# Kernel optimization log

Hardware: AMD Instinct MI355X
Metric: run time of the kernel (lower is better)

Reference implementation:

```python
import jax, jax.numpy as jnp
import numpy as np

V, E, HD, T, B, S = 32000, 256, 512, 9, 64, 512
H = HD // 2
PAD = 0
NEG = -10000.0


def setup_inputs() -> dict:
    key = jax.random.key(0)
    ks = jax.random.split(key, 12)
    # right-padded variable-length sequences (pack_padded_sequence semantics)
    lengths = jax.random.randint(ks[0], (B,), S // 4, S + 1)
    attention_mask = jnp.arange(S)[None, :] < lengths[:, None]  # [B,S] bool
    input_ids = jax.random.randint(ks[1], (B, S), 1, V)
    input_ids = jnp.where(attention_mask, input_ids, 0)
    sc = 1.0 / np.sqrt(H)
    embed_table = jax.random.normal(ks[2], (V, E), jnp.float32) * 0.02
    embed_table = embed_table.at[PAD].set(0.0)  # padding_idx=0
    u = lambda k, shp: jax.random.uniform(k, shp, jnp.float32, -sc, sc)
    Wih_f, Whh_f, b_f = u(ks[3], (4 * H, E)), u(ks[4], (4 * H, H)), u(ks[5], (4 * H,))
    Wih_r, Whh_r, b_r = u(ks[6], (4 * H, E)), u(ks[7], (4 * H, H)), u(ks[8], (4 * H,))
    W_out, b_out = u(ks[9], (T, HD)), u(ks[10], (T,))
    transitions = jax.random.normal(ks[11], (T, T), jnp.float32)
    transitions = transitions.at[PAD, :].set(NEG).at[:, PAD].set(NEG)
    return dict(input_ids=input_ids, attention_mask=attention_mask,
                embed_table=embed_table, Wih_f=Wih_f, Whh_f=Whh_f, b_f=b_f,
                Wih_r=Wih_r, Whh_r=Whh_r, b_r=b_r, W_out=W_out, b_out=b_out,
                transitions=transitions)


def _lstm_dir(x, m, Wih, Whh, b, reverse):
    """x: [S,B,E] time-major, m: [S,B] bool. Returns h outputs [S,B,H].
    Masked steps freeze (h,c), matching packed-sequence behavior for
    right-padded inputs in both scan directions."""
    Hh = Whh.shape[1]
    def step(carry, inp):
        h, c = carry
        xt, mt = inp
        g = xt @ Wih.T + h @ Whh.T + b                    # [B,4H]
        i, f, gg, o = jnp.split(g, 4, axis=-1)            # torch gate order i,f,g,o
        cn = jax.nn.sigmoid(f) * c + jax.nn.sigmoid(i) * jnp.tanh(gg)
        hn = jax.nn.sigmoid(o) * jnp.tanh(cn)
        mt = mt[:, None]
        return (jnp.where(mt, hn, h), jnp.where(mt, cn, c)), jnp.where(mt, hn, h)
    h0 = jnp.zeros((x.shape[1], Hh), x.dtype)
    _, hs = jax.lax.scan(step, (h0, h0), (x, m), reverse=reverse)
    return hs


def reference(input_ids, attention_mask, embed_table, Wih_f, Whh_f, b_f,
              Wih_r, Whh_r, b_r, W_out, b_out, transitions):
    mask = attention_mask.astype(bool)
    x = embed_table[input_ids].transpose(1, 0, 2)         # [S,B,E] time-major
    m = mask.T                                            # [S,B]
    hf = _lstm_dir(x, m, Wih_f, Whh_f, b_f, reverse=False)
    hr = _lstm_dir(x, m, Wih_r, Whh_r, b_r, reverse=True)
    hs = jnp.concatenate([hf, hr], axis=-1) * m[:, :, None]  # zero pads (pad_packed)
    feats = hs @ W_out.T + b_out                          # [S,B,T]
    # Viterbi forward pass
    v0 = jnp.full((feats.shape[1], T), NEG, feats.dtype).at[:, PAD].set(0.0)
    def vstep(v, inp):
        f_t, m_t = inp
        scores = v[:, :, None] + transitions[None]        # [B, from, to]
        bp = jnp.argmax(scores, axis=1)                   # [B,T]
        best = jnp.take_along_axis(scores, bp[:, None, :], axis=1)[:, 0, :] + f_t
        return jnp.where(m_t[:, None], best, v), bp
    v, bps = jax.lax.scan(vstep, v0, (feats, m))          # bps [S,B,T]
    last = jnp.argmax(v + transitions[PAD], axis=1)       # [B]
    # backtrace: path[i] = where(mask[i+1], bp[i+1][path[i+1]], 0)
    def bstep(tag, inp):
        bp_t, m_t = inp
        prev = jnp.take_along_axis(bp_t, tag[:, None], axis=1)[:, 0]
        prev = jnp.where(m_t, prev, 0)
        return prev, prev
    _, path_rest = jax.lax.scan(bstep, last, (bps[1:], m[1:]), reverse=True)
    return jnp.concatenate([path_rest, last[None]], axis=0).T  # [B,S]
```

## Files before the change

kernel.cpp:

```cpp
#include <hip/hip_runtime.h>


#define SLEN 512
#define NTAG 9
#define NEGV -10000.0f

typedef float f32x2 __attribute__((ext_vector_type(2)));
typedef float f32x4 __attribute__((ext_vector_type(4)));

__device__ __forceinline__ float qsum(float v){
  int t = __builtin_amdgcn_update_dpp(0, __float_as_int(v), 0xB1, 0xF, 0xF, false);
  v += __int_as_float(t);
  t = __builtin_amdgcn_update_dpp(0, __float_as_int(v), 0x4E, 0xF, 0xF, false);
  return v + __int_as_float(t);
}
__device__ __forceinline__ float rsum16(float v){
  v = qsum(v);
  int t = __builtin_amdgcn_update_dpp(0, __float_as_int(v), 0x124, 0xF, 0xF, false);
  v += __int_as_float(t);
  t = __builtin_amdgcn_update_dpp(0, __float_as_int(v), 0x128, 0xF, 0xF, false);
  return v + __int_as_float(t);
}

#define MAC2(S, WP, HV) { \
  f32x2 _h01{(HV).x,(HV).y}, _h23{(HV).z,(HV).w}; \
  asm("v_pk_fma_f32 %0, %1, %2, %0 op_sel:[0,0,0] op_sel_hi:[0,1,1]" : "+v"(S) : "v"(WP), "v"(_h01)); \
  asm("v_pk_fma_f32 %0, %1, %2, %0 op_sel:[1,0,0] op_sel_hi:[1,1,1]" : "+v"(S) : "v"(WP), "v"(_h23)); }

#define LDW(rr,kq,A,B) { f32x4 v = wp[((rr)*4+(kq))*1024 + t]; A = f32x2{v.x,v.y}; B = f32x2{v.z,v.w}; }

#define DECLW \
  f32x2 w00,w01,w02,w03,w04,w05,w06,w07; \
  f32x2 w10,w11,w12,w13,w14,w15,w16,w17; \
  f32x2 w20,w21,w22,w23,w24,w25,w26,w27; \
  f32x2 w30,w31,w32,w33,w34,w35,w36,w37; \
  LDW(0,0,w00,w01) LDW(0,1,w02,w03) LDW(0,2,w04,w05) LDW(0,3,w06,w07) \
  LDW(1,0,w10,w11) LDW(1,1,w12,w13) LDW(1,2,w14,w15) LDW(1,3,w16,w17) \
  LDW(2,0,w20,w21) LDW(2,1,w22,w23) LDW(2,2,w24,w25) LDW(2,3,w26,w27) \
  LDW(3,0,w30,w31) LDW(3,1,w32,w33) LDW(3,2,w34,w35) LDW(3,3,w36,w37)

#define PINW \
  asm volatile("" : "+v"(w00),"+v"(w01),"+v"(w02),"+v"(w03),"+v"(w04),"+v"(w05),"+v"(w06),"+v"(w07)); \
  asm volatile("" : "+v"(w10),"+v"(w11),"+v"(w12),"+v"(w13),"+v"(w14),"+v"(w15),"+v"(w16),"+v"(w17)); \
  asm volatile("" : "+v"(w20),"+v"(w21),"+v"(w22),"+v"(w23),"+v"(w24),"+v"(w25),"+v"(w26),"+v"(w27)); \
  asm volatile("" : "+v"(w30),"+v"(w31),"+v"(w32),"+v"(w33),"+v"(w34),"+v"(w35),"+v"(w36),"+v"(w37));

#define GCHUNK(c, WA0,WA1, WB0,WB1, WC0,WC1, WD0,WD1) { \
  f32x4 hA = *(const f32x4*)(hb + (c)*8); \
  f32x4 hB = *(const f32x4*)(hb + (c)*8 + 4); \
  MAC2(s0,WA0,hA) MAC2(s0,WA1,hB) \
  MAC2(s1,WB0,hA) MAC2(s1,WB1,hB) \
  MAC2(s2,WC0,hA) MAC2(s2,WC1,hB) \
  MAC2(s3,WD0,hA) MAC2(s3,WD1,hB) }

#define GEMV4x16 \
  f32x2 s0{0.f,0.f}, s1{0.f,0.f}, s2{0.f,0.f}, s3{0.f,0.f}; \
  GCHUNK(0, w00,w01, w10,w11, w20,w21, w30,w31) \
  GCHUNK(1, w02,w03, w12,w13, w22,w23, w32,w33) \
  GCHUNK(2, w04,w05, w14,w15, w24,w25, w34,w35) \
  GCHUNK(3, w06,w07, w16,w17, w26,w27, w36,w37)

union PK { struct { float v; int tg; } s; unsigned long long u; };

__global__ void prep_k(const float* __restrict__ wihf, const float* __restrict__ whhf,
                       const float* __restrict__ wihr, const float* __restrict__ whhr,
                       float* __restrict__ wS){
  for (int i = blockIdx.x*blockDim.x + threadIdx.x; i < (1<<20); i += gridDim.x*blockDim.x){
    int e=i&3, t=(i>>2)&1023, inst=(i>>12)&15, g=(i>>16)&3, d=(i>>18)&1, role=(i>>19)&1;
    int rr = inst>>2, kq = inst&3;
    int row = g*256 + (t>>4)*4 + rr;
    int k   = (t&15)*16 + kq*4 + e;
    const float* s = role ? (d? whhr : whhf) : (d? wihr : wihf);
    wS[i] = s[row*256 + k];
  }
}

__global__ __launch_bounds__(1024)
__attribute__((amdgpu_waves_per_eu(4,4)))
void xproj_k(
    int c0, int Sc,
    const int* __restrict__ ids, const float* __restrict__ embed,
    const float* __restrict__ wS,
    const float* __restrict__ bias_f, const float* __restrict__ bias_r,
    float* __restrict__ xg, long xg_par_str)
{
  __shared__ __align__(16) float xbig[64][576];
  __shared__ int ids_l[1024];
  const int t = threadIdx.x;
  const int bid = blockIdx.x;
  const int bp = bid & 31, g = (bid>>5)&3, d = bid>>7;
  const int rg = t>>4, ks = t&15;
  const int e = ks&3, bu = (ks>>2)&1;

  const f32x4* wp = (const f32x4*)(wS + (long)((d*4+g)*16)*4096);
  DECLW
  PINW
  const float bbr = (d ? bias_r : bias_f)[g*256 + rg*4 + e];

  for (int i=t; i<2*Sc; i+=1024){
    int b = (i>=Sc) ? 1 : 0, sp = i - b*Sc;
    int sg = d ? (SLEN-1-(c0*Sc+sp)) : (c0*Sc+sp);
    ids_l[i] = ids[(bp*2+b)*SLEN + sg];
  }
  const int SH = (Sc < 64) ? Sc : 64;
  float* xgb = xg + (long)(c0&1)*xg_par_str;

  for (int sp0=0; sp0<Sc; sp0+=SH){
    __syncthreads();
    for (int c = t; c < SH*128; c += 1024){
      int ss = c>>7, b = (c>>6)&1, kk = c&63;
      int sp = sp0 + ss;
      f32x4 v = ((const f32x4*)embed)[(long)ids_l[b*Sc+sp]*64 + kk];
      float* xb = &xbig[ss][(kk>>2)*36 + (kk&3)*8 + b];
      xb[0] = v.x; xb[2] = v.y; xb[4] = v.z; xb[6] = v.w;
    }
    __syncthreads();
    for (int sp=sp0; sp<sp0+SH; sp++){
      const float* hb = &xbig[sp-sp0][ks*36];
      GEMV4x16
      float r0a = rsum16(s0.x), r0b = rsum16(s0.y);
      float r1a = rsum16(s1.x), r1b = rsum16(s1.y);
      float r2a = rsum16(s2.x), r2b = rsum16(s2.y);
      float r3a = rsum16(s3.x), r3b = rsum16(s3.y);
      if (ks < 8){
        float va = (e==0)?r0a:(e==1)?r1a:(e==2)?r2a:r3a;
        float vb = (e==0)?r0b:(e==1)?r1b:(e==2)?r2b:r3b;
        long base = ((long)(d*Sc+sp)*64 + (bp*2+bu))*1024 + g*256 + rg*4 + e;
        xgb[base] = (bu ? vb : va) + bbr;
      }
    }
  }
}

__global__ __launch_bounds__(1024)
__attribute__((amdgpu_waves_per_eu(4,4)))
void recur_k(
    int c0, int Sc,
    const int* __restrict__ ids,
    const float* __restrict__ wS,
    const float* __restrict__ xg, long xg_par_str,
    float* __restrict__ hs,
    float* __restrict__ st_h, float* __restrict__ st_c,
    unsigned long long* __restrict__ send)
{
  __shared__ __align__(16) float hl2[2][576];
  __shared__ int ml[1024];
  const int t = threadIdx.x;
  const int bid = blockIdx.x;
  const int g = (bid>>3)&3;
  const int grp = (bid&7) | ((bid>>5)<<3);
  const int d = grp>>5, bp = grp&31;
  const int rg = t>>4, ks = t&15;
  const int e = ks&3, bu = (ks>>2)&1;
  const bool upd = (ks < 8);
  const int ju = rg*4 + e;
  const int bg = bp*2 + bu;

  const f32x4* wp = (const f32x4*)(wS + (long)(((2+d)*4+g)*16)*4096);
  DECLW
  PINW

  for (int i=t; i<2*Sc; i+=1024){
    int b = (i>=Sc) ? 1 : 0, sp = i - b*Sc;
    int sg = d ? (SLEN-1-(c0*Sc+sp)) : (c0*Sc+sp);
    ml[i] = ids[(bp*2+b)*SLEN + sg];
  }
  float cst = 0.f, hpv = 0.f;
  if (upd){
    hpv = st_h[(d*64+bg)*256 + ju];
    cst = st_c[(d*64+bg)*256 + ju];
    hl2[0][(ju>>4)*36 + (ju&15)*2 + bu] = hpv;
  }
  __syncthreads();
  const float* xgb = xg + (long)(c0&1)*xg_par_str;
  const int g1 = (g+1)&3, g2c = (g+2)&3, g3 = (g+3)&3;

  for (int sp=0; sp<Sc; sp++){
    const int stepg = c0*Sc + sp;
    const int par = stepg & 1;
    const int target = stepg + 1;
    float x0=0,x1=0,x2=0,x3=0;
    if (upd){
      const float* xr = xgb + ((long)(d*Sc+sp)*64 + bg)*1024 + ju;
      x0 = xr[0]; x1 = xr[256]; x2 = xr[512]; x3 = xr[768];
    }
    const float* hb = &hl2[sp&1][ks*36];
    GEMV4x16
    float r0a = rsum16(s0.x), r0b = rsum16(s0.y);
    float r1a = rsum16(s1.x), r1b = rsum16(s1.y);
    float r2a = rsum16(s2.x), r2b = rsum16(s2.y);
    float r3a = rsum16(s3.x), r3b = rsum16(s3.y);
    if (ks < 4){
      float ra = (ks==0)?r0a:(ks==1)?r1a:(ks==2)?r2a:r3a;
      float rb = (ks==0)?r0b:(ks==1)?r1b:(ks==2)?r2b:r3b;
      int j = rg*4 + ks;
      PK pa; pa.s.v = ra; pa.s.tg = target;
      PK pb; pb.s.v = rb; pb.s.tg = target;
      unsigned long long* sb = send + ((((long)(par*64+grp)*4 + g)*2)*256) + j;
      __hip_atomic_store(sb,       pa.u, __ATOMIC_RELAXED, __HIP_MEMORY_SCOPE_AGENT);
      __hip_atomic_store(sb + 256, pb.u, __ATOMIC_RELAXED, __HIP_MEMORY_SCOPE_AGENT);
    }
    if (upd){
      float voa = (e==0)?r0a:(e==1)?r1a:(e==2)?r2a:r3a;
      float vob = (e==0)?r0b:(e==1)?r1b:(e==2)?r2b:r3b;
      float vo  = bu ? vob : voa;
      const unsigned long long* rbase =
          send + (long)(par*64+grp)*4*2*256 + bu*256 + ju;
      PK u1, u2, u3;
      u1.u = __hip_atomic_load(rbase + (long)g1*512,  __ATOMIC_RELAXED, __HIP_MEMORY_SCOPE_AGENT);
      u2.u = __hip_atomic_load(rbase + (long)g2c*512, __ATOMIC_RELAXED, __HIP_MEMORY_SCOPE_AGENT);
      u3.u = __hip_atomic_load(rbase + (long)g3*512,  __ATOMIC_RELAXED, __HIP_MEMORY_SCOPE_AGENT);
      int cnt = 0;
      while (u1.s.tg < target || u2.s.tg < target || u3.s.tg < target){
        if (u1.s.tg < target) u1.u = __hip_atomic_load(rbase + (long)g1*512,  __ATOMIC_RELAXED, __HIP_MEMORY_SCOPE_AGENT);
        if (u2.s.tg < target) u2.u = __hip_atomic_load(rbase + (long)g2c*512, __ATOMIC_RELAXED, __HIP_MEMORY_SCOPE_AGENT);
        if (u3.s.tg < target) u3.u = __hip_atomic_load(rbase + (long)g3*512,  __ATOMIC_RELAXED, __HIP_MEMORY_SCOPE_AGENT);
        if (++cnt > (1<<15)) break;
      }
      float a0,a1,a2,a3;
      if      (g==0){ a0=vo;     a1=u1.s.v; a2=u2.s.v; a3=u3.s.v; }
      else if (g==1){ a1=vo;     a2=u1.s.v; a3=u2.s.v; a0=u3.s.v; }
      else if (g==2){ a2=vo;     a3=u1.s.v; a0=u2.s.v; a1=u3.s.v; }
      else          { a3=vo;     a0=u1.s.v; a1=u2.s.v; a2=u3.s.v; }
      float pi = a0 + x0, pf = a1 + x1, pg = a2 + x2, po = a3 + x3;
      float ii = 1.f/(1.f+expf(-pi)), ff = 1.f/(1.f+expf(-pf));
      float gv = tanhf(pg),           oo = 1.f/(1.f+expf(-po));
      float cn = ff*cst + ii*gv;
      float hn = oo*tanhf(cn);
      if (ml[bu*Sc+sp] != 0){ cst = cn; hpv = hn; }
      hl2[(sp+1)&1][(ju>>4)*36 + (ju&15)*2 + bu] = hpv;
      if (g == 0){
        int sg = d ? (SLEN-1-stepg) : stepg;
        hs[((long)sg*64 + bg)*512 + d*256 + ju] = hpv;
      }
    }
    __syncthreads();
  }
  if (upd){
    st_h[(d*64+bg)*256 + ju] = hpv;
    st_c[(d*64+bg)*256 + ju] = cst;
  }
}

__global__ __launch_bounds__(576) void feats_k(
    const float* __restrict__ hs, const float* __restrict__ wout,
    float* __restrict__ feats)
{
  __shared__ __align__(16) float hlds[64*512];
  __shared__ __align__(16) float wl[NTAG*512];
  const int s = blockIdx.x, t = threadIdx.x;
  for (int i = t; i < 64*512/4; i += 576)
    ((f32x4*)hlds)[i] = ((const f32x4*)(hs + (long)s*64*512))[i];
  for (int i = t; i < NTAG*512/4; i += 576)
    ((f32x4*)wl)[i] = ((const f32x4*)wout)[i];
  __syncthreads();
  int b = t / 9, tag = t - b*9;
  float acc = 0.f;
  const float* hb = hlds + b*512;
  const float* wb = wl + tag*512;
  for (int k=0; k<512; k+=4){
    f32x4 h4 = *(const f32x4*)(hb+k);
    f32x4 w4 = *(const f32x4*)(wb+k);
    acc += h4.x*w4.x + h4.y*w4.y + h4.z*w4.z + h4.w*w4.w;
  }
  feats[((long)s*64 + b)*9 + tag] = acc;
}

__global__ __launch_bounds__(64) void viterbi_k(
    const int* __restrict__ ids, const float* __restrict__ feats,
    const float* __restrict__ bout, const float* __restrict__ trans,
    int* __restrict__ outp)
{
  __shared__ float fl[SLEN*NTAG + 64];
  __shared__ unsigned char bps[SLEN*NTAG];
  __shared__ unsigned char mk[SLEN];
  const int b = blockIdx.x, lane = threadIdx.x;
  for (int i=lane; i<SLEN; i+=64) mk[i] = (ids[b*SLEN+i] != 0) ? 1 : 0;
  for (int i=lane; i<SLEN*NTAG; i+=64){
    int s = i/9; int t = i - s*9;
    fl[i] = feats[((long)s*64+b)*9 + t] + bout[t];
  }
  fl[SLEN*NTAG + lane] = 0.f;
  __syncthreads();

  float Tc[9], v[9], vown;
  #pragma unroll
  for (int i=0;i<9;i++) Tc[i] = (lane<9)? trans[i*9 + lane] : 0.f;
  #pragma unroll
  for (int i=0;i<9;i++) v[i] = (i==0)?0.f:NEGV;
  vown = (lane==0)?0.f:NEGV;

  for (int s=0;s<SLEN;s++){
    float best = v[0] + Tc[0]; int bi = 0;
    #pragma unroll
    for (int i=1;i<9;i++){
      float sc = v[i] + Tc[i];
      if (sc > best){ best = sc; bi = i; }
    }
    float nv = best + fl[s*9 + lane];
    bool m = mk[s] != 0;
    if (m && lane<9) vown = nv;
    if (lane < 9) bps[s*9+lane] = (unsigned char)bi;
    #pragma unroll
    for (int i=0;i<9;i++) v[i] = __shfl(vown, i);
  }
  if (lane == 0){
    float best = v[0]; int tag = 0;
    #pragma unroll
    for (int i=1;i<9;i++) if (v[i] > best){ best=v[i]; tag=i; }
    outp[b*SLEN + SLEN-1] = tag;
    for (int t=SLEN-1; t>=1; t--){
      int pv = bps[t*9 + tag];
      if (!mk[t]) pv = 0;
      outp[b*SLEN + t-1] = pv;
      tag = pv;
    }
  }
}

extern "C" void kernel_launch(void* const* d_in, const int* in_sizes, int n_in,
                              void* d_out, int out_size, void* d_ws, size_t ws_size,
                              hipStream_t stream){
  (void)in_sizes; (void)n_in; (void)out_size;
  const int*   ids   = (const int*)  d_in[0];
  const float* embed = (const float*)d_in[2];
  const float* Wih_f = (const float*)d_in[3];
  const float* Whh_f = (const float*)d_in[4];
  const float* b_f   = (const float*)d_in[5];
  const float* Wih_r = (const float*)d_in[6];
  const float* Whh_r = (const float*)d_in[7];
  const float* b_r   = (const float*)d_in[8];
  const float* Wout  = (const float*)d_in[9];
  const float* bout  = (const float*)d_in[10];
  const float* trans = (const float*)d_in[11];

  float* fw = (float*)d_ws;
  size_t off = 0;
  float* wS    = fw + off; off += 1048576;
  unsigned long long* send = (unsigned long long*)(fw + off); off += 524288;
  float* st_h  = fw + off; off += 32768;
  float* st_c  = fw + off; off += 32768;
  float* hs    = fw + off; off += 16777216;
  float* featb = fw + off; off += 294912;
  float* xg    = fw + off;
  size_t fixedB = off*4;

  const int cands[7] = {512,256,128,64,32,16,8};
  int Sc = 8;
  for (int ci=0; ci<7; ci++){
    size_t need = fixedB + (size_t)cands[ci]*262144*4;
    if (need <= ws_size){ Sc = cands[ci]; break; }
  }
  const long xg_par_str = (long)Sc*131072;
  const int C = SLEN / Sc;

  hipMemsetAsync(send, 0, 524288*4, stream);
  hipMemsetAsync(st_h, 0, 2*32768*4, stream);
  prep_k<<<1024,256,0,stream>>>(Wih_f, Whh_f, Wih_r, Whh_r, wS);
  for (int c0=0; c0<C; c0++){
    xproj_k<<<256,1024,0,stream>>>(c0, Sc, ids, embed, wS, b_f, b_r, xg, xg_par_str);
    recur_k<<<256,1024,0,stream>>>(c0, Sc, ids, wS, xg, xg_par_str, hs, st_h, st_c, send);
  }
  feats_k<<<512,576,0,stream>>>(hs, Wout, featb);
  viterbi_k<<<64,64,0,stream>>>(ids, featb, bout, trans, (int*)d_out);
}
```

Baseline: 2.273 ms.

## Fuse input projection and recurrence into one launch, overlapping chunks across block halves

The separate xproj and recurrence kernels are merged into a single kernel launched C+1 times. Blocks 0-127 run the recurrence for chunk Lx-1 while blocks 128-255 compute the input projection for chunk Lx, so projection work overlaps the serial recurrence. Each recurrence block now handles two batch-pair groups, which halves the number of recurrence blocks and runs two GEMVs per step. The aim is to hide projection time behind the recurrence and cut launch count, at the cost of more serial work per recurrence block and only 128 blocks pinning weights for each role.

```diff
diff --git a/kernel.cpp b/kernel.cpp
--- a/kernel.cpp
+++ b/kernel.cpp
@@ -75,170 +75,189 @@
   }
 }
 
+#define RECUR_GEMV_SEND(HL, GRP, OLP) { \
+  const float* hb = (HL) + ks*36; \
+  GEMV4x16 \
+  float r0a=rsum16(s0.x), r0b=rsum16(s0.y); \
+  float r1a=rsum16(s1.x), r1b=rsum16(s1.y); \
+  float r2a=rsum16(s2.x), r2b=rsum16(s2.y); \
+  float r3a=rsum16(s3.x), r3b=rsum16(s3.y); \
+  if (ks < 4){ \
+    float ra = (ks==0)?r0a:(ks==1)?r1a:(ks==2)?r2a:r3a; \
+    float rb = (ks==0)?r0b:(ks==1)?r1b:(ks==2)?r2b:r3b; \
+    int j = rg*4 + ks; \
+    (OLP)[j] = ra; (OLP)[256 + j] = rb; \
+    PK pa; pa.s.v = ra; pa.s.tg = target; \
+    PK pb; pb.s.v = rb; pb.s.tg = target; \
+    unsigned long long* sb = send + ((((long)(par*64+(GRP))*4 + g)*2)*256) + j; \
+    __hip_atomic_store(sb,       pa.u, __ATOMIC_RELAXED, __HIP_MEMORY_SCOPE_AGENT); \
+    __hip_atomic_store(sb + 256, pb.u, __ATOMIC_RELAXED, __HIP_MEMORY_SCOPE_AGENT); \
+  } }
+
+#define RECUR_UPD(GRP, OLP, HLW, HPV, CST, X0,X1,X2,X3, MLP, BGT) { \
+  const unsigned long long* rb_ = send + (long)(par*64+(GRP))*4*2*256 + b2*256 + j2; \
+  PK u1,u2,u3; \
+  u1.u = __hip_atomic_load(rb_ + (long)g1*512,  __ATOMIC_RELAXED, __HIP_MEMORY_SCOPE_AGENT); \
+  u2.u = __hip_atomic_load(rb_ + (long)g2c*512, __ATOMIC_RELAXED, __HIP_MEMORY_SCOPE_AGENT); \
+  u3.u = __hip_atomic_load(rb_ + (long)g3*512,  __ATOMIC_RELAXED, __HIP_MEMORY_SCOPE_AGENT); \
+  int cnt = 0; \
+  while (u1.s.tg < target || u2.s.tg < target || u3.s.tg < target){ \
+    if (u1.s.tg < target) u1.u = __hip_atomic_load(rb_ + (long)g1*512,  __ATOMIC_RELAXED, __HIP_MEMORY_SCOPE_AGENT); \
+    if (u2.s.tg < target) u2.u = __hip_atomic_load(rb_ + (long)g2c*512, __ATOMIC_RELAXED, __HIP_MEMORY_SCOPE_AGENT); \
+    if (u3.s.tg < target) u3.u = __hip_atomic_load(rb_ + (long)g3*512,  __ATOMIC_RELAXED, __HIP_MEMORY_SCOPE_AGENT); \
+    if (++cnt > (1<<15)) break; \
+  } \
+  float vo = (OLP)[b2*256 + j2]; \
+  float a0,a1,a2,a3; \
+  if      (g==0){ a0=vo; a1=u1.s.v; a2=u2.s.v; a3=u3.s.v; } \
+  else if (g==1){ a1=vo; a2=u1.s.v; a3=u2.s.v; a0=u3.s.v; } \
+  else if (g==2){ a2=vo; a3=u1.s.v; a0=u2.s.v; a1=u3.s.v; } \
+  else          { a3=vo; a0=u1.s.v; a1=u2.s.v; a2=u3.s.v; } \
+  float pi=a0+(X0), pf=a1+(X1), pg_=a2+(X2), po=a3+(X3); \
+  float ii=1.f/(1.f+expf(-pi)), ff=1.f/(1.f+expf(-pf)); \
+  float gv=tanhf(pg_), oo=1.f/(1.f+expf(-po)); \
+  float cn = ff*(CST) + ii*gv; \
+  float hn = oo*tanhf(cn); \
+  if ((MLP)[b2*Sc+sp] != 0){ (CST)=cn; (HPV)=hn; } \
+  (HLW)[(j2>>4)*36 + (j2&15)*2 + b2] = (HPV); \
+  if (g == 0){ \
+    int sg_ = d ? (SLEN-1-stepg) : stepg; \
+    hs[((long)sg_*64 + (BGT))*512 + d*256 + j2] = (HPV); \
+  } }
+
 __global__ __launch_bounds__(1024)
 __attribute__((amdgpu_waves_per_eu(4,4)))
-void xproj_k(
-    int c0, int Sc,
+void main_k(
+    int Lx, int C, int Sc,
     const int* __restrict__ ids, const float* __restrict__ embed,
     const float* __restrict__ wS,
     const float* __restrict__ bias_f, const float* __restrict__ bias_r,
-    float* __restrict__ xg, long xg_par_str)
-{
-  __shared__ __align__(16) float xbig[64][576];
-  __shared__ int ids_l[1024];
-  const int t = threadIdx.x;
-  const int bid = blockIdx.x;
-  const int bp = bid & 31, g = (bid>>5)&3, d = bid>>7;
-  const int rg = t>>4, ks = t&15;
-  const int e = ks&3, bu = (ks>>2)&1;
-
-  const f32x4* wp = (const f32x4*)(wS + (long)((d*4+g)*16)*4096);
-  DECLW
-  PINW
-  const float bbr = (d ? bias_r : bias_f)[g*256 + rg*4 + e];
-
-  for (int i=t; i<2*Sc; i+=1024){
-    int b = (i>=Sc) ? 1 : 0, sp = i - b*Sc;
-    int sg = d ? (SLEN-1-(c0*Sc+sp)) : (c0*Sc+sp);
-    ids_l[i] = ids[(bp*2+b)*SLEN + sg];
-  }
-  const int SH = (Sc < 64) ? Sc : 64;
-  float* xgb = xg + (long)(c0&1)*xg_par_str;
-
-  for (int sp0=0; sp0<Sc; sp0+=SH){
-    __syncthreads();
-    for (int c = t; c < SH*128; c += 1024){
-      int ss = c>>7, b = (c>>6)&1, kk = c&63;
-      int sp = sp0 + ss;
-      f32x4 v = ((const f32x4*)embed)[(long)ids_l[b*Sc+sp]*64 + kk];
-      float* xb = &xbig[ss][(kk>>2)*36 + (kk&3)*8 + b];
-      xb[0] = v.x; xb[2] = v.y; xb[4] = v.z; xb[6] = v.w;
-    }
-    __syncthreads();
-    for (int sp=sp0; sp<sp0+SH; sp++){
-      const float* hb = &xbig[sp-sp0][ks*36];
-      GEMV4x16
-      float r0a = rsum16(s0.x), r0b = rsum16(s0.y);
-      float r1a = rsum16(s1.x), r1b = rsum16(s1.y);
-      float r2a = rsum16(s2.x), r2b = rsum16(s2.y);
-      float r3a = rsum16(s3.x), r3b = rsum16(s3.y);
-      if (ks < 8){
-        float va = (e==0)?r0a:(e==1)?r1a:(e==2)?r2a:r3a;
-        float vb = (e==0)?r0b:(e==1)?r1b:(e==2)?r2b:r3b;
-        long base = ((long)(d*Sc+sp)*64 + (bp*2+bu))*1024 + g*256 + rg*4 + e;
-        xgb[base] = (bu ? vb : va) + bbr;
-      }
-    }
-  }
-}
-
-__global__ __launch_bounds__(1024)
-__attribute__((amdgpu_waves_per_eu(4,4)))
-void recur_k(
-    int c0, int Sc,
-    const int* __restrict__ ids,
-    const float* __restrict__ wS,
-    const float* __restrict__ xg, long xg_par_str,
+    float* __restrict__ xg, long xg_par_str,
     float* __restrict__ hs,
     float* __restrict__ st_h, float* __restrict__ st_c,
     unsigned long long* __restrict__ send)
 {
-  __shared__ __align__(16) float hl2[2][576];
-  __shared__ int ml[1024];
+  __shared__ __align__(16) float smem[64*576];
+  __shared__ int ids_l[1024];
   const int t = threadIdx.x;
   const int bid = blockIdx.x;
+
+  if (bid >= 128){
+    const int cx = Lx;
+    if (cx >= C) return;
+    const int x = bid - 128;
+    const int bq = x & 15, g = (x>>4)&3, d = x>>6;
+    const int rg = t>>4, ks = t&15;
+    const int e = ks&3, bu = (ks>>2)&1;
+    const f32x4* wp = (const f32x4*)(wS + (long)((d*4+g)*16)*4096);
+    DECLW
+    PINW
+    const float bbr = (d ? bias_r : bias_f)[g*256 + rg*4 + e];
+    float* xgb = xg + (long)(cx&1)*xg_par_str;
+    float (*xbig)[576] = (float(*)[576])smem;
+    const int SH = (Sc < 64) ? Sc : 64;
+
+    for (int pp=0; pp<2; pp++){
+      const int bp = bq*2 + pp;
+      for (int i=t; i<2*Sc; i+=1024){
+        int b = (i>=Sc) ? 1 : 0, sp = i - b*Sc;
+        int sg = d ? (SLEN-1-(cx*Sc+sp)) : (cx*Sc+sp);
+        ids_l[i] = ids[(bp*2+b)*SLEN + sg];
+      }
+      for (int sp0=0; sp0<Sc; sp0+=SH){
+        __syncthreads();
+        for (int c = t; c < SH*128; c += 1024){
+          int ss = c>>7, b = (c>>6)&1, kk = c&63;
+          int sp = sp0 + ss;
+          f32x4 v = ((const f32x4*)embed)[(long)ids_l[b*Sc+sp]*64 + kk];
+          float* xb = &xbig[ss][(kk>>2)*36 + (kk&3)*8 + b];
+          xb[0] = v.x; xb[2] = v.y; xb[4] = v.z; xb[6] = v.w;
+        }
+        __syncthreads();
+        for (int sp=sp0; sp<sp0+SH; sp++){
+          const float* hb = &xbig[sp-sp0][ks*36];
+          GEMV4x16
+          float r0a = rsum16(s0.x), r0b = rsum16(s0.y);
+          float r1a = rsum16(s1.x), r1b = rsum16(s1.y);
+          float r2a = rsum16(s2.x), r2b = rsum16(s2.y);
+          float r3a = rsum16(s3.x), r3b = rsum16(s3.y);
+          if (ks < 8){
+            float va = (e==0)?r0a:(e==1)?r1a:(e==2)?r2a:r3a;
+            float vb = (e==0)?r0b:(e==1)?r1b:(e==2)?r2b:r3b;
+            long base = ((long)(d*Sc+sp)*64 + (bp*2+bu))*1024 + g*256 + rg*4 + e;
+            xgb[base] = (bu ? vb : va) + bbr;
+          }
+        }
+      }
+      __syncthreads();
+    }
+    return;
+  }
+
+  const int cr = Lx - 1;
+  if (cr < 0) return;
   const int g = (bid>>3)&3;
-  const int grp = (bid&7) | ((bid>>5)<<3);
-  const int d = grp>>5, bp = grp&31;
+  const int grq = (bid&7) | ((bid>>5)<<3);
+  const int d = grq>>4, bq = grq&15;
   const int rg = t>>4, ks = t&15;
-  const int e = ks&3, bu = (ks>>2)&1;
-  const bool upd = (ks < 8);
-  const int ju = rg*4 + e;
-  const int bg = bp*2 + bu;
+  const int grp0 = d*32 + bq*2, grp1 = grp0 + 1;
+  const int g1 = (g+1)&3, g2c = (g+2)&3, g3 = (g+3)&3;
 
   const f32x4* wp = (const f32x4*)(wS + (long)(((2+d)*4+g)*16)*4096);
   DECLW
   PINW
 
-  for (int i=t; i<2*Sc; i+=1024){
-    int b = (i>=Sc) ? 1 : 0, sp = i - b*Sc;
-    int sg = d ? (SLEN-1-(c0*Sc+sp)) : (c0*Sc+sp);
-    ml[i] = ids[(bp*2+b)*SLEN + sg];
-  }
-  float cst = 0.f, hpv = 0.f;
-  if (upd){
-    hpv = st_h[(d*64+bg)*256 + ju];
-    cst = st_c[(d*64+bg)*256 + ju];
-    hl2[0][(ju>>4)*36 + (ju&15)*2 + bu] = hpv;
+  float* hl0 = smem;
+  float* hl1 = smem + 576;
+  float* ol  = smem + 1152;
+  int*   ml  = (int*)(smem + 2176);
+
+  for (int i=t; i<4*Sc; i+=1024){
+    int pp = (i >= 2*Sc) ? 1 : 0;
+    int ib = i - pp*2*Sc;
+    int b = (ib>=Sc) ? 1 : 0, sp = ib - b*Sc;
+    int sg = d ? (SLEN-1-(cr*Sc+sp)) : (cr*Sc+sp);
+    ml[i] = ids[(bq*4 + pp*2 + b)*SLEN + sg];
+  }
+  const int j2 = t&255, b2 = t>>8;
+  float hpv0=0.f, cst0=0.f, hpv1=0.f, cst1=0.f;
+  if (t < 512){
+    int bg0 = bq*4 + b2, bg1 = bq*4 + 2 + b2;
+    hpv0 = st_h[(d*64+bg0)*256 + j2]; cst0 = st_c[(d*64+bg0)*256 + j2];
+    hpv1 = st_h[(d*64+bg1)*256 + j2]; cst1 = st_c[(d*64+bg1)*256 + j2];
+    hl0[(j2>>4)*36 + (j2&15)*2 + b2] = hpv0;
+    hl1[(j2>>4)*36 + (j2&15)*2 + b2] = hpv1;
   }
   __syncthreads();
-  const float* xgb = xg + (long)(c0&1)*xg_par_str;
-  const int g1 = (g+1)&3, g2c = (g+2)&3, g3 = (g+3)&3;
+  const float* xgb = xg + (long)(cr&1)*xg_par_str;
 
   for (int sp=0; sp<Sc; sp++){
-    const int stepg = c0*Sc + sp;
+    const int stepg = cr*Sc + sp;
     const int par = stepg & 1;
     const int target = stepg + 1;
-    float x0=0,x1=0,x2=0,x3=0;
-    if (upd){
-      const float* xr = xgb + ((long)(d*Sc+sp)*64 + bg)*1024 + ju;
-      x0 = xr[0]; x1 = xr[256]; x2 = xr[512]; x3 = xr[768];
-    }
-    const float* hb = &hl2[sp&1][ks*36];
-    GEMV4x16
-    float r0a = rsum16(s0.x), r0b = rsum16(s0.y);
-    float r1a = rsum16(s1.x), r1b = rsum16(s1.y);
-    float r2a = rsum16(s2.x), r2b = rsum16(s2.y);
-    float r3a = rsum16(s3.x), r3b = rsum16(s3.y);
-    if (ks < 4){
-      float ra = (ks==0)?r0a:(ks==1)?r1a:(ks==2)?r2a:r3a;
-      float rb = (ks==0)?r0b:(ks==1)?r1b:(ks==2)?r2b:r3b;
-      int j = rg*4 + ks;
-      PK pa; pa.s.v = ra; pa.s.tg = target;
-      PK pb; pb.s.v = rb; pb.s.tg = target;
-      unsigned long long* sb = send + ((((long)(par*64+grp)*4 + g)*2)*256) + j;
-      __hip_atomic_store(sb,       pa.u, __ATOMIC_RELAXED, __HIP_MEMORY_SCOPE_AGENT);
-      __hip_atomic_store(sb + 256, pb.u, __ATOMIC_RELAXED, __HIP_MEMORY_SCOPE_AGENT);
-    }
-    if (upd){
-      float voa = (e==0)?r0a:(e==1)?r1a:(e==2)?r2a:r3a;
-      float vob = (e==0)?r0b:(e==1)?r1b:(e==2)?r2b:r3b;
-      float vo  = bu ? vob : voa;
-      const unsigned long long* rbase =
-          send + (long)(par*64+grp)*4*2*256 + bu*256 + ju;
-      PK u1, u2, u3;
-      u1.u = __hip_atomic_load(rbase + (long)g1*512,  __ATOMIC_RELAXED, __HIP_MEMORY_SCOPE_AGENT);
-      u2.u = __hip_atomic_load(rbase + (long)g2c*512, __ATOMIC_RELAXED, __HIP_MEMORY_SCOPE_AGENT);
-      u3.u = __hip_atomic_load(rbase + (long)g3*512,  __ATOMIC_RELAXED, __HIP_MEMORY_SCOPE_AGENT);
-      int cnt = 0;
-      while (u1.s.tg < target || u2.s.tg < target || u3.s.tg < target){
-        if (u1.s.tg < target) u1.u = __hip_atomic_load(rbase + (long)g1*512,  __ATOMIC_RELAXED, __HIP_MEMORY_SCOPE_AGENT);
-        if (u2.s.tg < target) u2.u = __hip_atomic_load(rbase + (long)g2c*512, __ATOMIC_RELAXED, __HIP_MEMORY_SCOPE_AGENT);
-        if (u3.s.tg < target) u3.u = __hip_atomic_load(rbase + (long)g3*512,  __ATOMIC_RELAXED, __HIP_MEMORY_SCOPE_AGENT);
-        if (++cnt > (1<<15)) break;
+    float x00=0,x01=0,x02=0,x03=0;
+    if (t < 512){
+      const float* xr = xgb + ((long)(d*Sc+sp)*64 + (bq*4+b2))*1024 + j2;
+      x00 = xr[0]; x01 = xr[256]; x02 = xr[512]; x03 = xr[768];
+    }
+    RECUR_GEMV_SEND(hl0, grp0, ol)
+    RECUR_GEMV_SEND(hl1, grp1, (ol+512))
+    __syncthreads();
+    if (t < 512){
+      RECUR_UPD(grp0, ol,       hl0, hpv0, cst0, x00,x01,x02,x03, ml,        (bq*4+b2))
+      float x10,x11,x12,x13;
+      {
+        const float* xr = xgb + ((long)(d*Sc+sp)*64 + (bq*4+2+b2))*1024 + j2;
+        x10 = xr[0]; x11 = xr[256]; x12 = xr[512]; x13 = xr[768];
       }
-      float a0,a1,a2,a3;
-      if      (g==0){ a0=vo;     a1=u1.s.v; a2=u2.s.v; a3=u3.s.v; }
-      else if (g==1){ a1=vo;     a2=u1.s.v; a3=u2.s.v; a0=u3.s.v; }
-      else if (g==2){ a2=vo;     a3=u1.s.v; a0=u2.s.v; a1=u3.s.v; }
-      else          { a3=vo;     a0=u1.s.v; a1=u2.s.v; a2=u3.s.v; }
-      float pi = a0 + x0, pf = a1 + x1, pg = a2 + x2, po = a3 + x3;
-      float ii = 1.f/(1.f+expf(-pi)), ff = 1.f/(1.f+expf(-pf));
-      float gv = tanhf(pg),           oo = 1.f/(1.f+expf(-po));
-      float cn = ff*cst + ii*gv;
-      float hn = oo*tanhf(cn);
-      if (ml[bu*Sc+sp] != 0){ cst = cn; hpv = hn; }
-      hl2[(sp+1)&1][(ju>>4)*36 + (ju&15)*2 + bu] = hpv;
-      if (g == 0){
-        int sg = d ? (SLEN-1-stepg) : stepg;
-        hs[((long)sg*64 + bg)*512 + d*256 + ju] = hpv;
-      }
+      RECUR_UPD(grp1, (ol+512), hl1, hpv1, cst1, x10,x11,x12,x13, (ml+2*Sc), (bq*4+2+b2))
     }
     __syncthreads();
   }
-  if (upd){
-    st_h[(d*64+bg)*256 + ju] = hpv;
-    st_c[(d*64+bg)*256 + ju] = cst;
+  if (t < 512){
+    int bg0 = bq*4 + b2, bg1 = bq*4 + 2 + b2;
+    st_h[(d*64+bg0)*256 + j2] = hpv0; st_c[(d*64+bg0)*256 + j2] = cst0;
+    st_h[(d*64+bg1)*256 + j2] = hpv1; st_c[(d*64+bg1)*256 + j2] = cst1;
   }
 }
 
@@ -357,9 +376,9 @@
   hipMemsetAsync(send, 0, 524288*4, stream);
   hipMemsetAsync(st_h, 0, 2*32768*4, stream);
   prep_k<<<1024,256,0,stream>>>(Wih_f, Whh_f, Wih_r, Whh_r, wS);
-  for (int c0=0; c0<C; c0++){
-    xproj_k<<<256,1024,0,stream>>>(c0, Sc, ids, embed, wS, b_f, b_r, xg, xg_par_str);
-    recur_k<<<256,1024,0,stream>>>(c0, Sc, ids, wS, xg, xg_par_str, hs, st_h, st_c, send);
+  for (int Lx=0; Lx<=C; Lx++){
+    main_k<<<256,1024,0,stream>>>(Lx, C, Sc, ids, embed, wS, b_f, b_r,
+                                  xg, xg_par_str, hs, st_h, st_c, send);
   }
   feats_k<<<512,576,0,stream>>>(hs, Wout, featb);
   viterbi_k<<<64,64,0,stream>>>(ids, featb, bout, trans, (int*)d_out);
```

New measurement: 2.429 ms. 6.9% more time.
